# Performance work log

Measured on AMD Instinct MI355X. Metric: run time of the kernel, lower is better.

Reference implementation:

```python
import jax, jax.numpy as jnp
import numpy as np

BLOCK = 32  # GGML quantization block size (Q4_0 style)
Q_OFFSET = 8.0  # 4-bit values stored unsigned in [0,16), centered by -8


def setup_inputs() -> dict:
    key = jax.random.key(0)
    k1, k2, k3, k4, k5, k6 = jax.random.split(key, 6)
    O, I, R, T = 4096, 4096, 16, 8192
    x = jax.random.normal(k1, (T, I), dtype=jnp.float32)
    qweight = jax.random.randint(k2, (O, I), 0, 16, dtype=jnp.int32)
    scales = jax.random.uniform(k3, (O, I // BLOCK), dtype=jnp.float32)
    lora_a = jax.random.normal(k4, (O, R), dtype=jnp.float32)
    lora_b = jax.random.normal(k5, (R, I), dtype=jnp.float32)
    bias = jax.random.normal(k6, (O,), dtype=jnp.float32)
    return {"x": x, "qweight": qweight, "scales": scales,
            "lora_a": lora_a, "lora_b": lora_b, "bias": bias}


def reference(x, qweight, scales, lora_a, lora_b, bias):
    # --- dequantize_tensor: per-block scale * centered int codes ---
    O, I = qweight.shape
    q = qweight.astype(jnp.float32) - Q_OFFSET            # [O, I]
    w = (q.reshape(O, I // BLOCK, BLOCK) * scales[:, :, None]).reshape(O, I)
    # --- patch application (LoRA-style additive patch) ---
    w = w + lora_a @ lora_b                               # [O, I]
    # --- downstream consumption: linear layer ---
    y = x @ w.T + bias                                    # [T, O]
    return y
```

## Files before the change

kernel.cpp:

```cpp
#include <hip/hip_runtime.h>
#include <hip/hip_bf16.h>

typedef unsigned short u16;
typedef __attribute__((ext_vector_type(4))) float f32x4;
typedef __attribute__((ext_vector_type(8))) short bf16x8;
typedef __attribute__((ext_vector_type(8))) u16 u16x8;

#define GLDS16(g, l) __builtin_amdgcn_global_load_lds( \
    (const __attribute__((address_space(1))) void*)(g), \
    (__attribute__((address_space(3))) void*)(l), 16, 0, 0)

__device__ inline u16 f2bf(float f) {
  union { float f; unsigned u; } v; v.f = f;
  unsigned r = v.u + 0x7fffu + ((v.u >> 16) & 1u);
  return (u16)(r >> 16);
}

__global__ __launch_bounds__(256) void k_dequant_lora(
    const int* __restrict__ qw, const float* __restrict__ sc,
    const float* __restrict__ la, const float* __restrict__ lb,
    u16* __restrict__ W)
{
  const int I = 4096, R = 16;
  __shared__ float lbs[16][512];
  __shared__ float las[256];
  const int c0 = blockIdx.x * 512;
  const int o0 = blockIdx.y * 16;
  const int tid = threadIdx.x;

  las[tid] = la[(size_t)(o0 + (tid >> 4)) * R + (tid & 15)];
  #pragma unroll
  for (int i = 0; i < 8; ++i) {
    int idx = tid + i * 256;
    int r = idx >> 7;
    int cc4 = (idx & 127) << 2;
    *(float4*)&lbs[r][cc4] = *(const float4*)&lb[(size_t)r * I + c0 + cc4];
  }
  __syncthreads();

  const int cc = (tid & 63) * 8;
  const int rg = tid >> 6;
  #pragma unroll
  for (int rr = 0; rr < 4; ++rr) {
    const int o = o0 + rg * 4 + rr;
    float acc[8] = {0.f,0.f,0.f,0.f,0.f,0.f,0.f,0.f};
    #pragma unroll
    for (int r = 0; r < 16; ++r) {
      float av = las[(rg * 4 + rr) * 16 + r];
      float4 b0 = *(const float4*)&lbs[r][cc];
      float4 b1 = *(const float4*)&lbs[r][cc + 4];
      acc[0] += av * b0.x; acc[1] += av * b0.y;
      acc[2] += av * b0.z; acc[3] += av * b0.w;
      acc[4] += av * b1.x; acc[5] += av * b1.y;
      acc[6] += av * b1.z; acc[7] += av * b1.w;
    }
    const int4* qp = (const int4*)&qw[(size_t)o * I + c0 + cc];
    int4 q0 = qp[0], q1 = qp[1];
    float s = sc[(size_t)o * (I / 32) + ((c0 + cc) >> 5)];
    u16x8 w;
    w[0] = f2bf(((float)q0.x - 8.0f) * s + acc[0]);
    w[1] = f2bf(((float)q0.y - 8.0f) * s + acc[1]);
    w[2] = f2bf(((float)q0.z - 8.0f) * s + acc[2]);
    w[3] = f2bf(((float)q0.w - 8.0f) * s + acc[3]);
    w[4] = f2bf(((float)q1.x - 8.0f) * s + acc[4]);
    w[5] = f2bf(((float)q1.y - 8.0f) * s + acc[5]);
    w[6] = f2bf(((float)q1.z - 8.0f) * s + acc[6]);
    w[7] = f2bf(((float)q1.w - 8.0f) * s + acc[7]);
    *(u16x8*)&W[(size_t)o * I + c0 + cc] = w;
  }
}

__global__ __launch_bounds__(256) void k_cvt(const float* __restrict__ x,
                                             u16* __restrict__ xb)
{
  const size_t n = (size_t)8192 * 4096;
  const size_t stride = (size_t)gridDim.x * 256 * 8;
  for (size_t i = ((size_t)blockIdx.x * 256 + threadIdx.x) * 8; i < n; i += stride) {
    float4 a = *(const float4*)&x[i];
    float4 b = *(const float4*)&x[i + 4];
    u16x8 o;
    o[0] = f2bf(a.x); o[1] = f2bf(a.y); o[2] = f2bf(a.z); o[3] = f2bf(a.w);
    o[4] = f2bf(b.x); o[5] = f2bf(b.y); o[6] = f2bf(b.z); o[7] = f2bf(b.w);
    *(u16x8*)&xb[i] = o;
  }
}

__global__ __launch_bounds__(512, 2) void k_gemm(
    const u16* __restrict__ A, const u16* __restrict__ B,
    const float* __restrict__ bias, float* __restrict__ C)
{
  const int N = 4096, K = 4096;
  const int NTK = 128;
  __shared__ u16 As[4 * 8192];
  __shared__ u16 Bs[4 * 8192];

  const int bid = blockIdx.x;
  const int swz = (bid & 7) * 64 + (bid >> 3);
  const int m0 = (swz >> 4) * 256;
  const int n0 = (swz & 15) * 256;

  const int tid = threadIdx.x;
  const int wid = tid >> 6, lane = tid & 63;
  const int wid_m = wid >> 2, wid_n = wid & 3;

  const int st0 = wid;
  const int st1 = 8 + wid;
  const int srow = lane >> 2;
  const int schunk = (((lane & 3) ^ (((lane >> 5) & 1) << 1))) * 8;
  const u16* Asrc0 = A + (size_t)(m0 + st0 * 16 + srow) * K + schunk;
  const u16* Asrc1 = A + (size_t)(m0 + st1 * 16 + srow) * K + schunk;
  const u16* Bsrc0 = B + (size_t)(n0 + st0 * 16 + srow) * K + schunk;
  const u16* Bsrc1 = B + (size_t)(n0 + st1 * 16 + srow) * K + schunk;

  #define STAGE_A(buf, t) do { \
    GLDS16(Asrc0 + (size_t)(t) * 32, &As[(buf) * 8192 + st0 * 512]); \
    GLDS16(Asrc1 + (size_t)(t) * 32, &As[(buf) * 8192 + st1 * 512]); } while (0)
  #define STAGE_B(buf, t) do { \
    GLDS16(Bsrc0 + (size_t)(t) * 32, &Bs[(buf) * 8192 + st0 * 512]); \
    GLDS16(Bsrc1 + (size_t)(t) * 32, &Bs[(buf) * 8192 + st1 * 512]); } while (0)

  const int LA = (lane & 15) * 32 + (((lane >> 4) * 8) ^ ((lane & 8) ? 16 : 0));
  const int wmb = wid_m * 8;
  const int wnb = wid_n * 4;

  f32x4 acc[8][4] = {};

  STAGE_A(0, 0); STAGE_B(0, 0);
  STAGE_A(1, 1); STAGE_B(1, 1);
  asm volatile("s_waitcnt vmcnt(4)" ::: "memory");
  __builtin_amdgcn_s_barrier();

  for (int t = 0; t < NTK; ++t) {
    const int b = t & 3;
    const u16* Ab = &As[b * 8192];
    const u16* Bb = &Bs[b * 8192];

    bf16x8 af[4], bfr[4];
    #pragma unroll
    for (int m = 0; m < 4; ++m)
      af[m] = *(const bf16x8*)&Ab[(wmb + m) * 512 + LA];
    #pragma unroll
    for (int n = 0; n < 4; ++n)
      bfr[n] = *(const bf16x8*)&Bb[(wnb + n) * 512 + LA];
    if (t + 2 < NTK) STAGE_A((t + 2) & 3, t + 2);
    __builtin_amdgcn_s_barrier();
    asm volatile("s_waitcnt lgkmcnt(0)" ::: "memory");
    __builtin_amdgcn_s_setprio(1);
    #pragma unroll
    for (int m = 0; m < 4; ++m)
      #pragma unroll
      for (int n = 0; n < 4; ++n)
        acc[m][n] = __builtin_amdgcn_mfma_f32_16x16x32_bf16(af[m], bfr[n], acc[m][n], 0, 0, 0);
    __builtin_amdgcn_s_setprio(0);
    __builtin_amdgcn_s_barrier();

    bf16x8 af2[4];
    #pragma unroll
    for (int m = 0; m < 4; ++m)
      af2[m] = *(const bf16x8*)&Ab[(wmb + 4 + m) * 512 + LA];
    if (t + 2 < NTK) {
      STAGE_B((t + 2) & 3, t + 2);
      asm volatile("s_waitcnt vmcnt(4)" ::: "memory");
    } else {
      asm volatile("s_waitcnt vmcnt(0)" ::: "memory");
    }
    __builtin_amdgcn_s_barrier();
    asm volatile("s_waitcnt lgkmcnt(0)" ::: "memory");
    __builtin_amdgcn_s_setprio(1);
    #pragma unroll
    for (int m = 0; m < 4; ++m)
      #pragma unroll
      for (int n = 0; n < 4; ++n)
        acc[4 + m][n] = __builtin_amdgcn_mfma_f32_16x16x32_bf16(af2[m], bfr[n], acc[4 + m][n], 0, 0, 0);
    __builtin_amdgcn_s_setprio(0);
    __builtin_amdgcn_s_barrier();
  }
  #undef STAGE_A
  #undef STAGE_B

  const int crow = m0 + wid_m * 128 + ((lane >> 4) << 2);
  const int ccol = n0 + wid_n * 64 + (lane & 15);
  #pragma unroll
  for (int n = 0; n < 4; ++n) {
    float bv = bias[ccol + n * 16];
    #pragma unroll
    for (int m = 0; m < 8; ++m) {
      #pragma unroll
      for (int j = 0; j < 4; ++j) {
        C[(size_t)(crow + m * 16 + j) * N + ccol + n * 16] = acc[m][n][j] + bv;
      }
    }
  }
}

extern "C" void kernel_launch(void* const* d_in, const int* in_sizes, int n_in,
                              void* d_out, int out_size, void* d_ws, size_t ws_size,
                              hipStream_t stream) {
  const float* x    = (const float*)d_in[0];
  const int*   qw   = (const int*)d_in[1];
  const float* sc   = (const float*)d_in[2];
  const float* la   = (const float*)d_in[3];
  const float* lb   = (const float*)d_in[4];
  const float* bias = (const float*)d_in[5];
  float* y = (float*)d_out;

  u16* W  = (u16*)d_ws;
  u16* Xb = (u16*)((char*)d_ws + (size_t)32 * 1024 * 1024);

  dim3 gridD(4096 / 512, 4096 / 16);
  k_dequant_lora<<<gridD, 256, 0, stream>>>(qw, sc, la, lb, W);
  k_cvt<<<2048, 256, 0, stream>>>(x, Xb);
  const int ngemm = (8192 / 256) * (4096 / 256);
  k_gemm<<<ngemm, 512, 0, stream>>>(Xb, W, bias, y);
}
```

Measured before the change: 372.0 us.

## Software-pipeline LDS fragment loads across k-tiles with register double buffering

Restructures the GEMM main loop so the next tile's A and B fragments are read from LDS while the current tile's second MFMA half runs. It uses ping-pong B fragment registers, unrolls by two, and drops two of the three barriers per k-step. sched_barrier calls pin the instruction order. This aims to hide LDS read latency and cut barrier stalls, at the cost of more registers and a riskier hazard argument about when a buffer is overwritten.

```diff
diff --git a/kernel.cpp b/kernel.cpp
--- a/kernel.cpp
+++ b/kernel.cpp
@@ -112,10 +112,10 @@
   const u16* Bsrc0 = B + (size_t)(n0 + st0 * 16 + srow) * K + schunk;
   const u16* Bsrc1 = B + (size_t)(n0 + st1 * 16 + srow) * K + schunk;
 
-  #define STAGE_A(buf, t) do { \
+#define STAGE_A(buf, t) do { \
     GLDS16(Asrc0 + (size_t)(t) * 32, &As[(buf) * 8192 + st0 * 512]); \
     GLDS16(Asrc1 + (size_t)(t) * 32, &As[(buf) * 8192 + st1 * 512]); } while (0)
-  #define STAGE_B(buf, t) do { \
+#define STAGE_B(buf, t) do { \
     GLDS16(Bsrc0 + (size_t)(t) * 32, &Bs[(buf) * 8192 + st0 * 512]); \
     GLDS16(Bsrc1 + (size_t)(t) * 32, &Bs[(buf) * 8192 + st1 * 512]); } while (0)
 
@@ -124,59 +124,72 @@
   const int wnb = wid_n * 4;
 
   f32x4 acc[8][4] = {};
+  bf16x8 aC[4], aN[4], bA[4], bB[4];
 
   STAGE_A(0, 0); STAGE_B(0, 0);
   STAGE_A(1, 1); STAGE_B(1, 1);
   asm volatile("s_waitcnt vmcnt(4)" ::: "memory");
   __builtin_amdgcn_s_barrier();
-
-  for (int t = 0; t < NTK; ++t) {
-    const int b = t & 3;
-    const u16* Ab = &As[b * 8192];
-    const u16* Bb = &Bs[b * 8192];
-
-    bf16x8 af[4], bfr[4];
-    #pragma unroll
-    for (int m = 0; m < 4; ++m)
-      af[m] = *(const bf16x8*)&Ab[(wmb + m) * 512 + LA];
-    #pragma unroll
-    for (int n = 0; n < 4; ++n)
-      bfr[n] = *(const bf16x8*)&Bb[(wnb + n) * 512 + LA];
-    if (t + 2 < NTK) STAGE_A((t + 2) & 3, t + 2);
-    __builtin_amdgcn_s_barrier();
-    asm volatile("s_waitcnt lgkmcnt(0)" ::: "memory");
-    __builtin_amdgcn_s_setprio(1);
-    #pragma unroll
-    for (int m = 0; m < 4; ++m)
-      #pragma unroll
-      for (int n = 0; n < 4; ++n)
-        acc[m][n] = __builtin_amdgcn_mfma_f32_16x16x32_bf16(af[m], bfr[n], acc[m][n], 0, 0, 0);
-    __builtin_amdgcn_s_setprio(0);
-    __builtin_amdgcn_s_barrier();
-
-    bf16x8 af2[4];
-    #pragma unroll
-    for (int m = 0; m < 4; ++m)
-      af2[m] = *(const bf16x8*)&Ab[(wmb + 4 + m) * 512 + LA];
-    if (t + 2 < NTK) {
-      STAGE_B((t + 2) & 3, t + 2);
-      asm volatile("s_waitcnt vmcnt(4)" ::: "memory");
-    } else {
-      asm volatile("s_waitcnt vmcnt(0)" ::: "memory");
-    }
-    __builtin_amdgcn_s_barrier();
-    asm volatile("s_waitcnt lgkmcnt(0)" ::: "memory");
-    __builtin_amdgcn_s_setprio(1);
-    #pragma unroll
-    for (int m = 0; m < 4; ++m)
-      #pragma unroll
-      for (int n = 0; n < 4; ++n)
-        acc[4 + m][n] = __builtin_amdgcn_mfma_f32_16x16x32_bf16(af2[m], bfr[n], acc[4 + m][n], 0, 0, 0);
-    __builtin_amdgcn_s_setprio(0);
-    __builtin_amdgcn_s_barrier();
-  }
-  #undef STAGE_A
-  #undef STAGE_B
+  __builtin_amdgcn_sched_barrier(0);
+  #pragma unroll
+  for (int m = 0; m < 4; ++m)
+    aC[m] = *(const bf16x8*)&As[(wmb + m) * 512 + LA];
+  #pragma unroll
+  for (int n = 0; n < 4; ++n)
+    bA[n] = *(const bf16x8*)&Bs[(wnb + n) * 512 + LA];
+
+#define TILE(T, BCUR, BNXT) do { \
+    const int b_ = (T) & 3; \
+    const int bn_ = ((T) + 1) & 3; \
+    _Pragma("unroll") \
+    for (int m = 0; m < 4; ++m) \
+      aN[m] = *(const bf16x8*)&As[b_ * 8192 + (wmb + 4 + m) * 512 + LA]; \
+    if ((T) + 2 < NTK) STAGE_A(((T) + 2) & 3, (T) + 2); \
+    __builtin_amdgcn_sched_barrier(0); \
+    __builtin_amdgcn_s_setprio(1); \
+    _Pragma("unroll") \
+    for (int m = 0; m < 4; ++m) { \
+      _Pragma("unroll") \
+      for (int n = 0; n < 4; ++n) \
+        acc[m][n] = __builtin_amdgcn_mfma_f32_16x16x32_bf16(aC[m], BCUR[n], acc[m][n], 0, 0, 0); \
+    } \
+    __builtin_amdgcn_s_setprio(0); \
+    __builtin_amdgcn_sched_barrier(0); \
+    if ((T) + 2 < NTK) { \
+      STAGE_B(((T) + 2) & 3, (T) + 2); \
+      asm volatile("s_waitcnt vmcnt(4)" ::: "memory"); \
+    } else { \
+      asm volatile("s_waitcnt vmcnt(0)" ::: "memory"); \
+    } \
+    __builtin_amdgcn_s_barrier(); \
+    __builtin_amdgcn_sched_barrier(0); \
+    if ((T) + 1 < NTK) { \
+      _Pragma("unroll") \
+      for (int m = 0; m < 4; ++m) \
+        aC[m] = *(const bf16x8*)&As[bn_ * 8192 + (wmb + m) * 512 + LA]; \
+      _Pragma("unroll") \
+      for (int n = 0; n < 4; ++n) \
+        BNXT[n] = *(const bf16x8*)&Bs[bn_ * 8192 + (wnb + n) * 512 + LA]; \
+    } \
+    __builtin_amdgcn_sched_barrier(0); \
+    __builtin_amdgcn_s_setprio(1); \
+    _Pragma("unroll") \
+    for (int m = 0; m < 4; ++m) { \
+      _Pragma("unroll") \
+      for (int n = 0; n < 4; ++n) \
+        acc[4 + m][n] = __builtin_amdgcn_mfma_f32_16x16x32_bf16(aN[m], BCUR[n], acc[4 + m][n], 0, 0, 0); \
+    } \
+    __builtin_amdgcn_s_setprio(0); \
+    __builtin_amdgcn_sched_barrier(0); \
+  } while (0)
+
+  for (int t = 0; t < NTK; t += 2) {
+    TILE(t, bA, bB);
+    TILE(t + 1, bB, bA);
+  }
+#undef TILE
+#undef STAGE_A
+#undef STAGE_B
 
   const int crow = m0 + wid_m * 128 + ((lane >> 4) << 2);
   const int ccol = n0 + wid_n * 64 + (lane & 15);
```

Measured after the change: 357.4 us. 1.04x faster.
